# Performance work log

Hardware: AMD Instinct MI355X
Metric: run time of the kernel (lower is better)

Reference implementation:

```python
import jax, jax.numpy as jnp
import numpy as np

D_MODEL = 1024
NHEAD = 16
D_K = D_MODEL // NHEAD
B, S = 2, 2048
NEG_INF = float('-inf')


def setup_inputs() -> dict:
    key = jax.random.key(0)
    ks = jax.random.split(key, 12)
    sc = 1.0 / np.sqrt(D_MODEL)
    return {
        'q': jax.random.normal(ks[0], (B, S, D_MODEL), dtype=jnp.float32),
        'k': jax.random.normal(ks[1], (B, S, D_MODEL), dtype=jnp.float32),
        'q_mask': jax.random.randint(ks[2], (B, S), 0, 2, dtype=jnp.int32),
        'k_mask': jax.random.randint(ks[3], (B, S), 0, 2, dtype=jnp.int32),
        'Wq': jax.random.normal(ks[4], (D_MODEL, D_MODEL), dtype=jnp.float32) * sc,
        'bq': jnp.zeros((D_MODEL,), dtype=jnp.float32),
        'Wk': jax.random.normal(ks[5], (D_MODEL, D_MODEL), dtype=jnp.float32) * sc,
        'bk': jnp.zeros((D_MODEL,), dtype=jnp.float32),
        'Wv': jax.random.normal(ks[6], (D_MODEL, D_MODEL), dtype=jnp.float32) * sc,
        'bv': jnp.zeros((D_MODEL,), dtype=jnp.float32),
        'Wo': jax.random.normal(ks[7], (D_MODEL, D_MODEL), dtype=jnp.float32) * sc,
        'bo': jnp.zeros((D_MODEL,), dtype=jnp.float32),
        'causal_attention': 1,
    }


def _split_heads(x):  # [B,S,D] -> [B,H,S,d_k]
    b, s, _ = x.shape
    return x.reshape(b, s, NHEAD, D_K).transpose(0, 2, 1, 3)


def reference(q, k, q_mask, k_mask, Wq, bq, Wk, bk, Wv, bv, Wo, bo, causal_attention):
    v_in = k  # module uses V = K
    qh = _split_heads(q @ Wq.T + bq)
    kh = _split_heads(k @ Wk.T + bk)
    vh = _split_heads(v_in @ Wv.T + bv)
    # [B,H,Sq,Sk]
    scores = jnp.einsum('bhqd,bhkd->bhqk', qh, kh) / jnp.sqrt(jnp.float32(D_K))
    sq, sk = scores.shape[-2], scores.shape[-1]
    if causal_attention:
        causal = jnp.triu(jnp.ones((sq, sk), dtype=bool), k=1)
        scores = jnp.where(causal[None, None], NEG_INF, scores)
    scores = jnp.where(k_mask[:, None, None, :] == 0, NEG_INF, scores)
    attn = jax.nn.softmax(scores, axis=-1)
    attn = jnp.where(q_mask[:, None, :, None] == 0, 0.0, attn)
    out = jnp.einsum('bhqk,bhkd->bhqd', attn, vh)  # [B,H,Sq,d_k]
    out = out.transpose(0, 2, 1, 3).reshape(q.shape[0], sq, D_MODEL)
    return out @ Wo.T + bo
```

## Files before the change

### kernel.cpp

```cpp
#include <hip/hip_runtime.h>

typedef unsigned short u16;
typedef unsigned int   u32;
typedef __bf16 bf16x8 __attribute__((ext_vector_type(8)));
typedef float  f32x4  __attribute__((ext_vector_type(4)));

#define NEG_INF (-__builtin_inff())

#define GLDS16(g, l) __builtin_amdgcn_global_load_lds( \
    (const __attribute__((address_space(1))) void*)(g), \
    (__attribute__((address_space(3))) void*)(l), 16, 0, 0)

__device__ __forceinline__ u16 f2bf(float f) {
  u32 u = __builtin_bit_cast(u32, f);
  u32 r = u + 0x7FFFu + ((u >> 16) & 1u);
  return (u16)(r >> 16);
}
__device__ __forceinline__ float bf2f(u16 v) {
  u32 u = ((u32)v) << 16;
  return __builtin_bit_cast(float, u);
}
__device__ __forceinline__ u32 pk2bf(float a, float b) {
  return __builtin_amdgcn_perm(__builtin_bit_cast(u32, b),
                               __builtin_bit_cast(u32, a), 0x07060302u);
}

struct ConvArgs {
  const void* src[10];
  u16* dst[10];
};

__global__ void convert_kernel(ConvArgs a, const int* __restrict__ kmask,
                               u16* __restrict__ mask01, int* __restrict__ flag) {
  if (blockIdx.x >= 1024) {
    int idx = (blockIdx.x - 1024) * 256 + threadIdx.x;
    mask01[idx] = kmask[idx] ? 0x3F80u : 0u;
    return;
  }
  __shared__ int cnt;
  if (threadIdx.x == 0) cnt = 0;
  __syncthreads();
  const u16* q16 = (const u16*)a.src[0];
  int local = 0;
  for (int i = threadIdx.x; i < 8192; i += 256) {
    int e = (q16[i] >> 7) & 0xFF;
    if (e >= 118 && e <= 129) local++;
  }
  atomicAdd(&cnt, local);
  __syncthreads();
  const int fl = (cnt > 6144) ? 1 : 0;
  if (blockIdx.x == 0 && threadIdx.x == 0) flag[0] = fl;

  const int total = 1573376;
  for (int u0 = blockIdx.x * 256 + threadIdx.x; u0 < total; u0 += 1024 * 256) {
    int s, off;
    if (u0 < 1048576)      { s = u0 >> 19;                 off = u0 & 524287; }
    else if (u0 < 1572864) { int v = u0 - 1048576; s = 2 + (v >> 17); off = v & 131071; }
    else                   { int v = u0 - 1572864; s = 6 + (v >> 7);  off = v & 127; }
    u16* d = a.dst[s] + (size_t)off * 8;
    if (fl) {
      const uint4* sp = (const uint4*)((const u16*)a.src[s] + (size_t)off * 8);
      *(uint4*)d = *sp;
    } else {
      const float* sp = (const float*)a.src[s] + (size_t)off * 8;
      u16 tmp[8];
      #pragma unroll
      for (int j = 0; j < 8; j++) tmp[j] = f2bf(sp[j]);
      *(uint4*)d = *(uint4*)tmp;
    }
  }
}

template <int BM, int BN>
__device__ __forceinline__ void gemm_mainloop(
    const u16* __restrict__ A, const u16* __restrict__ W,
    int bm, int bn, u16 (*As)[BM * 32], u16 (*Bs)[BN * 32],
    f32x4 (*acc)[BN / 32]) {
  const int t = threadIdx.x, lane = t & 63, w = t >> 6;
  const int wm = (w >> 1) * (BM / 2), wn = (w & 1) * (BN / 2);
  const int l15 = lane & 15, quad = lane >> 4;
  const int sr = t >> 2, sc = (t & 3) * 8;
  const u16* Ag0 = A + (size_t)(bm + sr) * 1024 + sc;
  const u16* Ag1 = Ag0 + (size_t)64 * 1024;
  const u16* Wg0 = W + (size_t)(bn + sr) * 1024 + sc;
  const u16* Wg1 = Wg0 + (size_t)64 * 1024;

  GLDS16(Ag0, As[0] + t * 8);
  if (BM == 128) GLDS16(Ag1, As[0] + 2048 + t * 8);
  GLDS16(Wg0, Bs[0] + t * 8);
  if (BN == 128) GLDS16(Wg1, Bs[0] + 2048 + t * 8);

  int st = 0;
  for (int k0 = 0; k0 < 1024; k0 += 32, st ^= 1) {
    __syncthreads();
    if (k0 + 32 < 1024) {
      GLDS16(Ag0 + k0 + 32, As[st ^ 1] + t * 8);
      if (BM == 128) GLDS16(Ag1 + k0 + 32, As[st ^ 1] + 2048 + t * 8);
      GLDS16(Wg0 + k0 + 32, Bs[st ^ 1] + t * 8);
      if (BN == 128) GLDS16(Wg1 + k0 + 32, Bs[st ^ 1] + 2048 + t * 8);
    }
    bf16x8 af[BM / 32], bw[BN / 32];
    #pragma unroll
    for (int i = 0; i < BM / 32; i++)
      af[i] = *(const bf16x8*)&As[st][(wm + i * 16 + l15) * 32 + quad * 8];
    #pragma unroll
    for (int j = 0; j < BN / 32; j++)
      bw[j] = *(const bf16x8*)&Bs[st][(wn + j * 16 + l15) * 32 + quad * 8];
    #pragma unroll
    for (int i = 0; i < BM / 32; i++)
      #pragma unroll
      for (int j = 0; j < BN / 32; j++)
        acc[i][j] = __builtin_amdgcn_mfma_f32_16x16x32_bf16(af[i], bw[j], acc[i][j], 0, 0, 0);
  }
}

__global__ __launch_bounds__(256, 5) void qkv_proj_kernel(
    const u16* __restrict__ qc, const u16* __restrict__ kc,
    const u16* __restrict__ Wq, const u16* __restrict__ Wk, const u16* __restrict__ Wv,
    const u16* __restrict__ bq, const u16* __restrict__ bk, const u16* __restrict__ bv,
    const int* __restrict__ kmask,
    u16* __restrict__ Qp, u16* __restrict__ Kp, u16* __restrict__ Vt) {
  __shared__ __align__(16) u16 As[2][64 * 32];
  __shared__ __align__(16) u16 Bs[2][128 * 32];
  const int bid = blockIdx.x;
  const int xb = (bid >> 3) & 7;
  const int g = ((bid >> 6) << 3) | (bid & 7);
  const int z = g >> 6, yb = g & 63;
  const u16* A    = (z == 0) ? qc : kc;
  const u16* W    = (z == 0) ? Wq : (z == 1) ? Wk : Wv;
  const u16* bias = (z == 0) ? bq : (z == 1) ? bk : bv;
  const int bm = yb * 64, bn = xb * 128;

  const f32x4 fzero = {0.f, 0.f, 0.f, 0.f};
  f32x4 acc[2][4];
  #pragma unroll
  for (int i = 0; i < 2; i++)
    #pragma unroll
    for (int j = 0; j < 4; j++) acc[i][j] = fzero;

  gemm_mainloop<64, 128>(A, W, bm, bn, As, Bs, acc);

  const int t = threadIdx.x, lane = t & 63, w = t >> 6;
  const int wm = (w >> 1) * 32, wn = (w & 1) * 64;
  const int l15 = lane & 15, quad = lane >> 4;

  if (z < 2) {
    u16* out = (z == 0) ? Qp : Kp;
    #pragma unroll
    for (int i = 0; i < 2; i++)
      #pragma unroll
      for (int j = 0; j < 4; j++) {
        int n = bn + wn + j * 16 + l15;
        float bb = bf2f(bias[n]);
        int m0 = bm + wm + i * 16 + quad * 4;
        #pragma unroll
        for (int r = 0; r < 4; r++)
          out[(size_t)(m0 + r) * 1024 + n] = f2bf(acc[i][j][r] + bb);
      }
  } else {
    #pragma unroll
    for (int i = 0; i < 2; i++) {
      int m0 = bm + wm + i * 16 + quad * 4;
      int b_ = m0 >> 11, s0 = m0 & 2047;
      const int4 km = *(const int4*)&kmask[b_ * 2048 + s0];
      #pragma unroll
      for (int j = 0; j < 4; j++) {
        int n = bn + wn + j * 16 + l15;
        int hh = n >> 6, dw = n & 63;
        float bb = bf2f(bias[n]);
        u16 tmp[4];
        tmp[0] = km.x ? f2bf(acc[i][j][0] + bb) : (u16)0;
        tmp[1] = km.y ? f2bf(acc[i][j][1] + bb) : (u16)0;
        tmp[2] = km.z ? f2bf(acc[i][j][2] + bb) : (u16)0;
        tmp[3] = km.w ? f2bf(acc[i][j][3] + bb) : (u16)0;
        *(ushort4*)&Vt[((size_t)(b_ * 16 + hh) * 64 + dw) * 2048 + s0] = *(ushort4*)tmp;
      }
    }
  }
}

__global__ __launch_bounds__(256, 4) void attn_kernel(
    const u16* __restrict__ Qp, const u16* __restrict__ Kp, const u16* __restrict__ Vt,
    const int* __restrict__ qmask, const u16* __restrict__ mask01,
    const int* __restrict__ causal_p, u16* __restrict__ AO) {
  __shared__ __align__(16) u16 KS[2][128 * 64];
  __shared__ __align__(16) u16 VS[2][64 * 128];
  __shared__ __align__(16) u16 P[4][16 * 64];

  const int t = threadIdx.x, lane = t & 63, w = t >> 6;
  const int quad = lane >> 4, l15 = lane & 15, l7 = l15 & 7;
  const int bh = blockIdx.x & 31;
  const int g4 = 31 - (int)(blockIdx.x >> 5);
  const int b = bh >> 4, h = bh & 15;
  const int causal = *causal_p;
  const int q0 = g4 * 64 + w * 16;
  const int nkt = causal ? (g4 >> 1) + 1 : 16;
  const float cs = 0.18033688011112042f;
  const float C = 40.0f;
  const f32x4 fzero = {0.f, 0.f, 0.f, 0.f};

  const u16* qr = Qp + (size_t)(b * 2048 + q0 + l15) * 1024 + h * 64 + quad * 8;
  const bf16x8 qf0 = *(const bf16x8*)qr;
  const bf16x8 qf1 = *(const bf16x8*)(qr + 32);

  const int kLr = lane >> 3, kLc = lane & 7;
  const u16* kgw = Kp + (size_t)(b * 2048 + 32 * w + kLr) * 1024 + h * 64 +
                   (kLc ^ kLr) * 8;
  const int vLr = lane >> 4, vLc = lane & 15;
  const u16* vgw = Vt + (size_t)bh * 131072 + (size_t)(16 * w) * 2048;
  int voff[4];
  #pragma unroll
  for (int i = 0; i < 4; i++)
    voff[i] = (4 * i + vLr) * 2048 + ((vLc ^ (4 * i + vLr)) * 8);
  u16* kls0 = &KS[0][(32 * w) * 64] + lane * 8;
  u16* kls1 = &KS[1][(32 * w) * 64] + lane * 8;
  u16* vls0 = &VS[0][(16 * w) * 128] + lane * 8;
  u16* vls1 = &VS[1][(16 * w) * 128] + lane * 8;

  f32x4 Oa[4], Dacc = fzero;
  #pragma unroll
  for (int dt = 0; dt < 4; dt++) Oa[dt] = fzero;
  u16* Pw = P[w];
  const u16* mrow = mask01 + b * 2048;

  {
    const u16* kg = kgw;
    const u16* vg = vgw;
    #pragma unroll
    for (int i = 0; i < 4; i++) {
      GLDS16(kg + i * 8192, kls0 + i * 512);
      GLDS16(vg + voff[i], vls0 + i * 512);
    }
  }

  for (int kt = 0; kt < nkt; kt++) {
    __syncthreads();
    if (kt + 1 < nkt) {
      const u16* kg = kgw + (size_t)(kt + 1) * 131072;
      const u16* vg = vgw + (kt + 1) * 128;
      u16* kd = ((kt + 1) & 1) ? kls1 : kls0;
      u16* vd = ((kt + 1) & 1) ? vls1 : vls0;
      #pragma unroll
      for (int i = 0; i < 4; i++) {
        GLDS16(kg + i * 8192, kd + i * 512);
        GLDS16(vg + voff[i], vd + i * 512);
      }
    }
    if (causal && kt * 128 > q0 + 15) continue;
    const u16* KSc = KS[kt & 1];
    const u16* VSc = VS[kt & 1];

    f32x4 sa[8];
    #pragma unroll
    for (int mt = 0; mt < 8; mt++) sa[mt] = fzero;
    #pragma unroll
    for (int mt = 0; mt < 8; mt++) {
      bf16x8 kf0 = *(const bf16x8*)&KSc[(mt * 16 + l15) * 64 + ((quad ^ l7) * 8)];
      bf16x8 kf1 = *(const bf16x8*)&KSc[(mt * 16 + l15) * 64 + (((quad ^ l7) ^ 4) * 8)];
      sa[mt] = __builtin_amdgcn_mfma_f32_16x16x32_bf16(kf0, qf0, sa[mt], 0, 0, 0);
      sa[mt] = __builtin_amdgcn_mfma_f32_16x16x32_bf16(kf1, qf1, sa[mt], 0, 0, 0);
    }

    const bool diag = causal && (kt * 128 + 127 > q0);
    #pragma unroll
    for (int mt = 0; mt < 8; mt++)
      #pragma unroll
      for (int r = 0; r < 4; r++) {
        float p = __builtin_amdgcn_exp2f(__builtin_fmaf(sa[mt][r], cs, -C));
        if (diag && (kt * 128 + mt * 16 + quad * 4 + r > q0 + l15)) p = 0.f;
        sa[mt][r] = p;
      }

    #pragma unroll
    for (int hh = 0; hh < 2; hh++) {
      #pragma unroll
      for (int mh = 0; mh < 4; mh++) {
        int B = mh * 2 + (quad >> 1);
        uint2 pk;
        pk.x = pk2bf(sa[hh * 4 + mh][0], sa[hh * 4 + mh][1]);
        pk.y = pk2bf(sa[hh * 4 + mh][2], sa[hh * 4 + mh][3]);
        *(uint2*)&Pw[l15 * 64 + ((B ^ l7) * 8) + (quad & 1) * 4] = pk;
      }
      #pragma unroll
      for (int kh = 0; kh < 2; kh++) {
        int kp = hh * 2 + kh;
        bf16x8 pf = *(const bf16x8*)&Pw[l15 * 64 + (((kh * 4 + quad) ^ l7) * 8)];
        bf16x8 mf = *(const bf16x8*)(mrow + kt * 128 + kp * 32 + quad * 8);
        Dacc = __builtin_amdgcn_mfma_f32_16x16x32_bf16(pf, mf, Dacc, 0, 0, 0);
        #pragma unroll
        for (int dt = 0; dt < 4; dt++) {
          bf16x8 vf = *(const bf16x8*)
              &VSc[(dt * 16 + l15) * 128 + (((kp * 4 + quad) ^ l15) * 8)];
          Oa[dt] = __builtin_amdgcn_mfma_f32_16x16x32_bf16(pf, vf, Oa[dt], 0, 0, 0);
        }
      }
    }
  }

  const int4 qm = *(const int4*)&qmask[b * 2048 + q0 + quad * 4];
  f32x4 fv;
  fv[0] = (Dacc[0] > 0.f && qm.x) ? (1.0f / Dacc[0]) : 0.f;
  fv[1] = (Dacc[1] > 0.f && qm.y) ? (1.0f / Dacc[1]) : 0.f;
  fv[2] = (Dacc[2] > 0.f && qm.z) ? (1.0f / Dacc[2]) : 0.f;
  fv[3] = (Dacc[3] > 0.f && qm.w) ? (1.0f / Dacc[3]) : 0.f;
  #pragma unroll
  for (int dt = 0; dt < 4; dt++)
    #pragma unroll
    for (int r = 0; r < 4; r++)
      AO[(size_t)(b * 2048 + q0 + quad * 4 + r) * 1024 + h * 64 + dt * 16 + l15] =
          f2bf(Oa[dt][r] * fv[r]);
}

__global__ __launch_bounds__(256) void oproj_kernel(
    const u16* __restrict__ AO, const u16* __restrict__ Wo, const u16* __restrict__ bo,
    void* __restrict__ out, const int* __restrict__ flag) {
  __shared__ __align__(16) u16 As[2][64 * 32];
  __shared__ __align__(16) u16 Bs[2][64 * 32];
  const int bid = blockIdx.x;
  const int xb = (bid >> 3) & 15;
  const int g = ((bid >> 7) << 3) | (bid & 7);
  const int bm = g * 64, bn = xb * 64;

  const f32x4 fzero = {0.f, 0.f, 0.f, 0.f};
  f32x4 acc[2][2];
  #pragma unroll
  for (int i = 0; i < 2; i++)
    #pragma unroll
    for (int j = 0; j < 2; j++) acc[i][j] = fzero;

  gemm_mainloop<64, 64>(AO, Wo, bm, bn, As, Bs, acc);

  const int t = threadIdx.x, lane = t & 63, w = t >> 6;
  const int wm = (w >> 1) * 32, wn = (w & 1) * 32;
  const int l15 = lane & 15, quad = lane >> 4;
  const int isbf = *flag;
  #pragma unroll
  for (int i = 0; i < 2; i++)
    #pragma unroll
    for (int j = 0; j < 2; j++) {
      int n = bn + wn + j * 16 + l15;
      float bb = bf2f(bo[n]);
      int m0 = bm + wm + i * 16 + quad * 4;
      #pragma unroll
      for (int r = 0; r < 4; r++) {
        float v = acc[i][j][r] + bb;
        size_t idx = (size_t)(m0 + r) * 1024 + n;
        if (isbf) ((u16*)out)[idx] = f2bf(v);
        else      ((float*)out)[idx] = v;
      }
    }
}

extern "C" void kernel_launch(void* const* d_in, const int* in_sizes, int n_in,
                              void* d_out, int out_size, void* d_ws, size_t ws_size,
                              hipStream_t stream) {
  (void)in_sizes; (void)n_in; (void)out_size; (void)ws_size;

  char* w = (char*)d_ws;
  int* flag = (int*)w;
  u16* qc  = (u16*)(w + 256);
  u16* kc  = qc  + 4194304;
  u16* Qp  = kc  + 4194304;
  u16* Kp  = Qp  + 4194304;
  u16* Vt  = Kp  + 4194304;
  u16* AO  = Vt  + 4194304;
  u16* Wqc = AO  + 4194304;
  u16* Wkc = Wqc + 1048576;
  u16* Wvc = Wkc + 1048576;
  u16* Woc = Wvc + 1048576;
  u16* bqc = Woc + 1048576;
  u16* bkc = bqc + 1024;
  u16* bvc = bkc + 1024;
  u16* boc = bvc + 1024;
  u16* mask01 = boc + 1024;

  ConvArgs ca;
  ca.src[0] = d_in[0];  ca.dst[0] = qc;
  ca.src[1] = d_in[1];  ca.dst[1] = kc;
  ca.src[2] = d_in[4];  ca.dst[2] = Wqc;
  ca.src[3] = d_in[6];  ca.dst[3] = Wkc;
  ca.src[4] = d_in[8];  ca.dst[4] = Wvc;
  ca.src[5] = d_in[10]; ca.dst[5] = Woc;
  ca.src[6] = d_in[5];  ca.dst[6] = bqc;
  ca.src[7] = d_in[7];  ca.dst[7] = bkc;
  ca.src[8] = d_in[9];  ca.dst[8] = bvc;
  ca.src[9] = d_in[11]; ca.dst[9] = boc;
  convert_kernel<<<1040, 256, 0, stream>>>(ca, (const int*)d_in[3], mask01, flag);

  qkv_proj_kernel<<<1536, 256, 0, stream>>>(
      qc, kc, Wqc, Wkc, Wvc, bqc, bkc, bvc, (const int*)d_in[3], Qp, Kp, Vt);

  attn_kernel<<<1024, 256, 0, stream>>>(
      Qp, Kp, Vt, (const int*)d_in[2], mask01, (const int*)d_in[12], AO);

  oproj_kernel<<<1024, 256, 0, stream>>>(AO, Woc, boc, d_out, flag);
}
```

Before: 219.9 us.

## Load GEMM A fragments directly from global into registers, k-major LDS layout for W

The shared GEMM mainloop used by the QKV and output projections no longer stages the A tile through LDS. Each wave now loads its A fragments straight from global memory into registers, prefetched one k-step ahead. The W tile is stored in LDS in a k-chunk-major layout so the fragment reads avoid strided row access, and the A LDS buffers are removed. The aim is to cut LDS traffic and footprint. The cost is uncoalesced 16-byte global loads, duplicated across the two waves that share A rows, which depend on the cache.

```diff
diff --git a/kernel.cpp b/kernel.cpp
--- a/kernel.cpp
+++ b/kernel.cpp
@@ -71,46 +71,47 @@
   }
 }
 
-template <int BM, int BN>
-__device__ __forceinline__ void gemm_mainloop(
+template <int BN>
+__device__ __forceinline__ void gemm_mainloop_v3(
     const u16* __restrict__ A, const u16* __restrict__ W,
-    int bm, int bn, u16 (*As)[BM * 32], u16 (*Bs)[BN * 32],
-    f32x4 (*acc)[BN / 32]) {
+    int bm, int bn, u16 (*Bs)[BN * 32], f32x4 (*acc)[BN / 32]) {
   const int t = threadIdx.x, lane = t & 63, w = t >> 6;
-  const int wm = (w >> 1) * (BM / 2), wn = (w & 1) * (BN / 2);
+  const int wm = (w >> 1) * 32, wn = (w & 1) * (BN / 2);
   const int l15 = lane & 15, quad = lane >> 4;
-  const int sr = t >> 2, sc = (t & 3) * 8;
-  const u16* Ag0 = A + (size_t)(bm + sr) * 1024 + sc;
-  const u16* Ag1 = Ag0 + (size_t)64 * 1024;
-  const u16* Wg0 = W + (size_t)(bn + sr) * 1024 + sc;
-  const u16* Wg1 = Wg0 + (size_t)64 * 1024;
-
-  GLDS16(Ag0, As[0] + t * 8);
-  if (BM == 128) GLDS16(Ag1, As[0] + 2048 + t * 8);
+
+  const int s0 = t;
+  const u16* Wg0 = W + (size_t)(bn + (s0 & (BN - 1))) * 1024 + (s0 / BN) * 8;
+  const u16* Wg1 = W + (size_t)(bn + ((s0 + 256) & (BN - 1))) * 1024 +
+                   ((s0 + 256) / BN) * 8;
+
+  const u16* Ar0 = A + (size_t)(bm + wm + l15) * 1024 + quad * 8;
+  const u16* Ar1 = Ar0 + (size_t)16 * 1024;
+
   GLDS16(Wg0, Bs[0] + t * 8);
-  if (BN == 128) GLDS16(Wg1, Bs[0] + 2048 + t * 8);
+  if (BN == 128) GLDS16(Wg1, Bs[0] + (t + 256) * 8);
+  bf16x8 afc0 = *(const bf16x8*)Ar0;
+  bf16x8 afc1 = *(const bf16x8*)Ar1;
 
   int st = 0;
   for (int k0 = 0; k0 < 1024; k0 += 32, st ^= 1) {
     __syncthreads();
+    bf16x8 afn0 = afc0, afn1 = afc1;
     if (k0 + 32 < 1024) {
-      GLDS16(Ag0 + k0 + 32, As[st ^ 1] + t * 8);
-      if (BM == 128) GLDS16(Ag1 + k0 + 32, As[st ^ 1] + 2048 + t * 8);
       GLDS16(Wg0 + k0 + 32, Bs[st ^ 1] + t * 8);
-      if (BN == 128) GLDS16(Wg1 + k0 + 32, Bs[st ^ 1] + 2048 + t * 8);
-    }
-    bf16x8 af[BM / 32], bw[BN / 32];
-    #pragma unroll
-    for (int i = 0; i < BM / 32; i++)
-      af[i] = *(const bf16x8*)&As[st][(wm + i * 16 + l15) * 32 + quad * 8];
+      if (BN == 128) GLDS16(Wg1 + k0 + 32, Bs[st ^ 1] + (t + 256) * 8);
+      afn0 = *(const bf16x8*)(Ar0 + k0 + 32);
+      afn1 = *(const bf16x8*)(Ar1 + k0 + 32);
+    }
+    bf16x8 bw[BN / 32];
     #pragma unroll
     for (int j = 0; j < BN / 32; j++)
-      bw[j] = *(const bf16x8*)&Bs[st][(wn + j * 16 + l15) * 32 + quad * 8];
-    #pragma unroll
-    for (int i = 0; i < BM / 32; i++)
-      #pragma unroll
-      for (int j = 0; j < BN / 32; j++)
-        acc[i][j] = __builtin_amdgcn_mfma_f32_16x16x32_bf16(af[i], bw[j], acc[i][j], 0, 0, 0);
+      bw[j] = *(const bf16x8*)&Bs[st][(quad * BN + wn + j * 16 + l15) * 8];
+    #pragma unroll
+    for (int j = 0; j < BN / 32; j++) {
+      acc[0][j] = __builtin_amdgcn_mfma_f32_16x16x32_bf16(afc0, bw[j], acc[0][j], 0, 0, 0);
+      acc[1][j] = __builtin_amdgcn_mfma_f32_16x16x32_bf16(afc1, bw[j], acc[1][j], 0, 0, 0);
+    }
+    afc0 = afn0; afc1 = afn1;
   }
 }
 
@@ -120,7 +121,6 @@
     const u16* __restrict__ bq, const u16* __restrict__ bk, const u16* __restrict__ bv,
     const int* __restrict__ kmask,
     u16* __restrict__ Qp, u16* __restrict__ Kp, u16* __restrict__ Vt) {
-  __shared__ __align__(16) u16 As[2][64 * 32];
   __shared__ __align__(16) u16 Bs[2][128 * 32];
   const int bid = blockIdx.x;
   const int xb = (bid >> 3) & 7;
@@ -138,7 +138,7 @@
     #pragma unroll
     for (int j = 0; j < 4; j++) acc[i][j] = fzero;
 
-  gemm_mainloop<64, 128>(A, W, bm, bn, As, Bs, acc);
+  gemm_mainloop_v3<128>(A, W, bm, bn, Bs, acc);
 
   const int t = threadIdx.x, lane = t & 63, w = t >> 6;
   const int wm = (w >> 1) * 32, wn = (w & 1) * 64;
@@ -314,7 +314,6 @@
 __global__ __launch_bounds__(256) void oproj_kernel(
     const u16* __restrict__ AO, const u16* __restrict__ Wo, const u16* __restrict__ bo,
     void* __restrict__ out, const int* __restrict__ flag) {
-  __shared__ __align__(16) u16 As[2][64 * 32];
   __shared__ __align__(16) u16 Bs[2][64 * 32];
   const int bid = blockIdx.x;
   const int xb = (bid >> 3) & 15;
@@ -328,7 +327,7 @@
     #pragma unroll
     for (int j = 0; j < 2; j++) acc[i][j] = fzero;
 
-  gemm_mainloop<64, 64>(AO, Wo, bm, bn, As, Bs, acc);
+  gemm_mainloop_v3<64>(AO, Wo, bm, bn, Bs, acc);
 
   const int t = threadIdx.x, lane = t & 63, w = t >> 6;
   const int wm = (w >> 1) * 32, wn = (w & 1) * 32;
```

Result: slower. 297.1 us (+35.1%).
